# Kernel tuning notes

Hardware: AMD Instinct MI355X
Metric: run time of the kernel (lower is better)

The kernel has to match this reference:

```python
import jax, jax.numpy as jnp
import numpy as np

# ---- module constants (from init_kwargs) ----
VOXEL_SIZE = np.array([0.1, 0.1, 0.2], np.float32)
PC_RANGE = np.array([0.0, -40.0, -3.0, 70.4, 40.0, 1.0], np.float32)
MAX_PTS = 10            # max_points_in_voxel
MAX_VOX = 40000         # max_voxel_num (hard voxelization cap per sample)
GRID = np.round((PC_RANGE[3:] - PC_RANGE[:3]) / VOXEL_SIZE).astype(np.int32)  # [704,800,20] (x,y,z)
BIG = int(GRID[0]) * int(GRID[1]) * int(GRID[2])

PC_MIN = jnp.asarray(PC_RANGE[:3])
VSIZE = jnp.asarray(VOXEL_SIZE)
GRID_J = jnp.asarray(GRID)

B = 8
N_PER_B = 120000


def setup_inputs() -> dict:
    key = jax.random.key(0)
    k1, = jax.random.split(key, 1)
    u = jax.random.uniform(k1, (B * N_PER_B, 4), dtype=jnp.float32)
    # place points inside (and slightly around) pc_range
    x = u[:, 0] * 72.0 - 0.5
    y = u[:, 1] * 82.0 - 41.0
    z = u[:, 2] * 4.4 - 3.2
    inten = u[:, 3]
    bs_idx = jnp.repeat(jnp.arange(B, dtype=jnp.float32), N_PER_B)
    points = jnp.stack([bs_idx, x, y, z, inten], axis=1)  # [960000, 5]
    return {"points": points, "batch_size": B}


def _voxelize_one(pts):
    """Hard voxelization of one point cloud pts [N,4] -> fixed-size buffers.
    Faithful to first-come voxel ordering and per-voxel point caps."""
    N = pts.shape[0]
    idxs = jnp.arange(N, dtype=jnp.int32)
    xyz = pts[:, :3]
    c = jnp.floor((xyz - PC_MIN) / VSIZE).astype(jnp.int32)  # [N,3] (x,y,z)
    valid = jnp.all((c >= 0) & (c < GRID_J), axis=1)
    lid = (c[:, 2] * GRID[1] + c[:, 1]) * GRID[0] + c[:, 0]  # z-major linear id
    lid = jnp.where(valid, lid, BIG)

    order = jnp.argsort(lid)            # stable: within a voxel, original order kept
    lid_s = lid[order]
    is_new = jnp.concatenate([jnp.ones((1,), bool), lid_s[1:] != lid_s[:-1]])
    gid = jnp.cumsum(is_new.astype(jnp.int32)) - 1           # group id per sorted point
    starts = jax.lax.cummax(jnp.where(is_new, idxs, 0))      # group start position
    pos = idxs - starts                                      # rank inside its voxel

    g_lid = jax.ops.segment_min(lid_s, gid, num_segments=N)
    g_valid = g_lid < BIG
    first_orig = jax.ops.segment_min(order.astype(jnp.int32), gid, num_segments=N)
    # voxel slot = first-appearance rank (invalid/empty groups pushed to the end)
    first_key = jnp.where(g_valid, first_orig, N + idxs)
    perm = jnp.argsort(first_key)
    slot = jnp.zeros(N, jnp.int32).at[perm].set(idxs)

    pslot = slot[gid]
    keep = g_valid[gid] & (pslot < MAX_VOX) & (pos < MAX_PTS)
    sslot = jnp.where(keep, pslot, MAX_VOX)   # overflow bucket, sliced off
    spos = jnp.where(keep, pos, 0)
    voxels = jnp.zeros((MAX_VOX + 1, MAX_PTS, pts.shape[1]), pts.dtype)
    voxels = voxels.at[sslot, spos].set(pts[order])[:MAX_VOX]

    gcount = jax.ops.segment_sum(keep.astype(jnp.int32), gid, num_segments=N)
    gslot = jnp.where(g_valid & (slot < MAX_VOX), slot, MAX_VOX)
    num_points = jnp.zeros(MAX_VOX + 1, jnp.int32).at[gslot].set(gcount)[:MAX_VOX]

    cs = c[order]
    gz = jax.ops.segment_min(cs[:, 2], gid, num_segments=N)
    gy = jax.ops.segment_min(cs[:, 1], gid, num_segments=N)
    gx = jax.ops.segment_min(cs[:, 0], gid, num_segments=N)
    coors = jnp.full((MAX_VOX + 1, 3), -1, jnp.int32)
    coors = coors.at[gslot].set(jnp.stack([gz, gy, gx], axis=1))[:MAX_VOX]  # (z,y,x)
    return voxels, num_points, coors


def reference(points, batch_size):
    feats = points[:, 1:]
    n_per_b = feats.shape[0] // batch_size  # points constructed contiguously per sample
    pts = feats.reshape(batch_size, n_per_b, feats.shape[1])
    voxels_b, num_b, coors_b = jax.vmap(_voxelize_one)(pts)
    voxels = voxels_b.reshape(batch_size * MAX_VOX, MAX_PTS, feats.shape[1])
    num_points = num_b.reshape(-1)
    batch_col = jnp.repeat(jnp.arange(batch_size, dtype=jnp.int32), MAX_VOX)[:, None]
    coors_batch = jnp.concatenate([batch_col, coors_b.reshape(-1, 3)], axis=1)  # [b,z,y,x]
    grid_size = jnp.asarray(GRID)
    return voxels, num_points, coors_batch, grid_size
```

## Files before the change

### kernel.cpp

```cpp
#include <hip/hip_runtime.h>

#define NB        8
#define NPB       120000
#define NPTS      (NB * NPB)
#define MAX_PTS   10
#define MAX_VOX   40000
#define GX        704
#define GY        800
#define GZ        20
#define CELLS     (GX * GY * GZ)

#define HC2       (1 << 18)
#define HMASK2    (HC2 - 1)
#define NSLOT2    (NB * HC2)

#define TILES     469
#define TILES_PAD 512
#define MBCAP     8192
#define MTILE     2048

#define EMPTY64   0xFFFFFFFFFFFFFFFFull

#define OUT_VOX   0LL
#define OUT_NUM   12800000LL
#define OUT_COOR  13120000LL
#define OUT_GRID  14400000LL

__device__ __forceinline__ bool point_cell(const float* __restrict__ p,
                                           int& cx, int& cy, int& cz) {
    cx = (int)floorf((p[1] - 0.0f)   / 0.1f);
    cy = (int)floorf((p[2] - (-40.0f)) / 0.1f);
    cz = (int)floorf((p[3] - (-3.0f))  / 0.2f);
    return (cx >= 0) & (cx < GX) & (cy >= 0) & (cy < GY) & (cz >= 0) & (cz < GZ);
}

__device__ __forceinline__ unsigned cell_hash(int lid) {
    return (((unsigned)lid * 2654435761u) >> 14) & HMASK2;
}

__global__ void k_init(float* __restrict__ out, ulonglong2* __restrict__ slab2,
                       uint4* __restrict__ flag4, unsigned* __restrict__ mcount) {
    int t = blockIdx.x * blockDim.x + threadIdx.x;
    int stride = gridDim.x * blockDim.x;
    ulonglong2 e2; e2.x = EMPTY64; e2.y = EMPTY64;
    for (int i = t; i < NSLOT2 / 2; i += stride) slab2[i] = e2;
    uint4 z4 = make_uint4(0u, 0u, 0u, 0u);
    for (int i = t; i < NPTS / 16; i += stride) flag4[i] = z4;
    if (t < NB) mcount[t * 16] = 0u;
    if (t == 0) {
        out[OUT_GRID + 0] = 704.f;
        out[OUT_GRID + 1] = 800.f;
        out[OUT_GRID + 2] = 20.f;
    }
}

__global__ void k_insert(const float* __restrict__ pts,
                         unsigned long long* __restrict__ slabB,
                         int* __restrict__ lid32) {
    int b = blockIdx.x & 7;
    int idx = (blockIdx.x >> 3) * 256 + threadIdx.x;
    if (idx >= NPB) return;
    int g = b * NPB + idx;
    const float* p = pts + (long long)g * 5;
    int cx, cy, cz;
    if (!point_cell(p, cx, cy, cz)) { lid32[g] = -1; return; }
    int lid = (cz * GY + cy) * GX + cx;
    lid32[g] = lid;
    unsigned h = cell_hash(lid);
    unsigned long long key = ((unsigned long long)(unsigned)lid << 32)
                           | (unsigned long long)(unsigned)idx;
    unsigned long long* base = slabB + (size_t)b * HC2;
    while (true) {
        unsigned long long old = atomicMin(base + h, key);
        if (old == EMPTY64) break;
        if ((old >> 32) == (key >> 32)) break;
        if (old > key) key = old;
        h = (h + 1) & HMASK2;
    }
}

__global__ void k_mark(const ulonglong2* __restrict__ slab2,
                       unsigned char* __restrict__ flag) {
    int b = blockIdx.x & 7;
    int i = (blockIdx.x >> 3) * 256 + threadIdx.x;
    ulonglong2 v = slab2[(size_t)b * (HC2 / 2) + i];
    if (v.x != EMPTY64) flag[b * NPB + (unsigned)v.x] = 1;
    if (v.y != EMPTY64) flag[b * NPB + (unsigned)v.y] = 1;
}

__global__ void k_rankscan(const unsigned char* __restrict__ flag,
                           unsigned char* __restrict__ rank8, int* __restrict__ tileSum) {
    int b = blockIdx.x & 7;
    int tile = blockIdx.x >> 3;
    int idx = tile * 256 + threadIdx.x;
    int f = 0;
    if (idx < NPB) f = flag[b * NPB + idx];
    __shared__ int sc[256];
    sc[threadIdx.x] = f;
    __syncthreads();
    for (int off = 1; off < 256; off <<= 1) {
        int v = sc[threadIdx.x];
        if ((int)threadIdx.x >= off) v += sc[threadIdx.x - off];
        __syncthreads();
        sc[threadIdx.x] = v;
        __syncthreads();
    }
    if (idx < NPB) rank8[b * NPB + idx] = (unsigned char)(sc[threadIdx.x] - f);
    if (threadIdx.x == 255) tileSum[b * TILES_PAD + tile] = sc[255];
}

__global__ void k_finish(const float* __restrict__ pts, const int* __restrict__ lid32,
                         const unsigned char* __restrict__ flag,
                         const unsigned char* __restrict__ rank8,
                         const int* __restrict__ tileSum,
                         const unsigned long long* __restrict__ slabB,
                         float* __restrict__ out, int2* __restrict__ mlist,
                         unsigned* __restrict__ mcount) {
    int b = blockIdx.x & 7;
    int tile = blockIdx.x >> 3;
    int t = threadIdx.x;

    __shared__ int sc[256];
    __shared__ int soff[TILES_PAD];
    int v0 = (2 * t     < TILES) ? tileSum[b * TILES_PAD + 2 * t]     : 0;
    int v1 = (2 * t + 1 < TILES) ? tileSum[b * TILES_PAD + 2 * t + 1] : 0;
    int w = v0 + v1;
    sc[t] = w;
    __syncthreads();
    for (int off = 1; off < 256; off <<= 1) {
        int x = sc[t];
        if (t >= off) x += sc[t - off];
        __syncthreads();
        sc[t] = x;
        __syncthreads();
    }
    int e = sc[t] - w;
    soff[2 * t] = e;
    soff[2 * t + 1] = e + v0;
    __syncthreads();

    int idx = tile * 256 + t;
    if (idx >= NPB) return;
    int g = b * NPB + idx;
    int lid = lid32[g];
    if (lid < 0) return;

    if (flag[g]) {
        int slot = soff[idx >> 8] + (int)rank8[g];
        if (slot >= MAX_VOX) return;
        unsigned ul = (unsigned)lid;
        unsigned cx = ul % (unsigned)GX;
        unsigned tt = ul / (unsigned)GX;
        unsigned cy = tt % (unsigned)GY;
        unsigned cz = tt / (unsigned)GY;
        long long r = (long long)b * MAX_VOX + slot;
        ((float4*)(out + OUT_COOR))[r] = make_float4((float)b, (float)cz, (float)cy, (float)cx);
        out[OUT_NUM + r] = 1.f;
        const float* p = pts + (long long)g * 5;
        float4* row = (float4*)(out + OUT_VOX + r * (MAX_PTS * 4));
        row[0] = make_float4(p[1], p[2], p[3], p[4]);
        float4 zf = make_float4(0.f, 0.f, 0.f, 0.f);
        #pragma unroll
        for (int i = 1; i < MAX_PTS; i++) row[i] = zf;
    } else {
        const unsigned long long* base = slabB + (size_t)b * HC2;
        unsigned h = cell_hash(lid);
        unsigned long long cur;
        while (true) {
            cur = base[h];
            if ((unsigned)(cur >> 32) == (unsigned)lid) break;
            h = (h + 1) & HMASK2;
        }
        unsigned minidx = (unsigned)cur;
        int slot = soff[(int)minidx >> 8] + (int)rank8[b * NPB + (int)minidx];
        if (slot >= MAX_VOX) return;
        unsigned m = atomicAdd(&mcount[b * 16], 1u);
        if (m < MBCAP) mlist[(size_t)b * MBCAP + m] = make_int2(slot, idx);
    }
}

__global__ void k_multi(const float* __restrict__ pts,
                        const int2* __restrict__ mlist, const unsigned* __restrict__ mcount,
                        float* __restrict__ out) {
    int b = blockIdx.y;
    unsigned n = mcount[b * 16];
    if (n > MBCAP) n = MBCAP;
    unsigned t = blockIdx.x * blockDim.x + threadIdx.x;
    const int2* lst = mlist + (size_t)b * MBCAP;
    bool active = (t < n);
    int2 e = active ? lst[t] : make_int2(-1, -1);
    int pos = 1;
    int same = 0;
    __shared__ int2 sm[MTILE];
    for (unsigned chunk = 0; chunk < n; chunk += MTILE) {
        unsigned m = n - chunk;
        if (m > MTILE) m = MTILE;
        for (unsigned i = threadIdx.x; i < m; i += 256)
            sm[i] = lst[chunk + i];
        __syncthreads();
        if (active) {
            #pragma unroll 4
            for (unsigned j = 0; j < m; j++) {
                int2 o = sm[j];
                if (o.x == e.x) { same++; if (o.y < e.y) pos++; }
            }
        }
        __syncthreads();
    }
    if (!active) return;
    if (pos == 1) {
        int cnt = same + 1;
        out[OUT_NUM + (long long)b * MAX_VOX + e.x] =
            (float)(cnt < MAX_PTS ? cnt : MAX_PTS);
    }
    if (pos >= MAX_PTS) return;
    const float* p = pts + ((long long)b * NPB + e.y) * 5;
    ((float4*)(out + OUT_VOX))[(long long)(b * MAX_VOX + e.x) * MAX_PTS + pos] =
        make_float4(p[1], p[2], p[3], p[4]);
}

extern "C" void kernel_launch(void* const* d_in, const int* in_sizes, int n_in,
                              void* d_out, int out_size, void* d_ws, size_t ws_size,
                              hipStream_t stream) {
    const float* pts = (const float*)d_in[0];
    float* out = (float*)d_out;

    char* w = (char*)d_ws;
    unsigned long long* slabB = (unsigned long long*)w;
    w += (size_t)NSLOT2 * 8;
    unsigned char* flag = (unsigned char*)w;  w += (size_t)NPTS;
    unsigned char* rank8 = (unsigned char*)w; w += (size_t)NPTS;
    int* lid32 = (int*)w;    w += (size_t)NPTS * 4;
    int* tileSum = (int*)w;  w += (size_t)NB * TILES_PAD * 4;
    int2* mlist = (int2*)w;  w += (size_t)NB * MBCAP * 8;
    unsigned* mcount = (unsigned*)w; w += (size_t)NB * 16 * 4;

    const int PB = TILES * NB;
    k_init<<<dim3(2048), dim3(256), 0, stream>>>(out, (ulonglong2*)slabB, (uint4*)flag, mcount);
    k_insert<<<dim3(PB), dim3(256), 0, stream>>>(pts, slabB, lid32);
    k_mark<<<dim3(NB * (HC2 / 2 / 256)), dim3(256), 0, stream>>>((const ulonglong2*)slabB, flag);
    k_rankscan<<<dim3(PB), dim3(256), 0, stream>>>(flag, rank8, tileSum);
    k_finish<<<dim3(PB), dim3(256), 0, stream>>>(pts, lid32, flag, rank8, tileSum, slabB, out, mlist, mcount);
    k_multi<<<dim3(MBCAP / 256, NB), dim3(256), 0, stream>>>(pts, mlist, mcount, out);
}
```

Baseline: 174.1 us.

## Mark first-of-voxel flags during insert and fold rank scan into finish

Flags start at one, and the hash-insert kernel clears the flag of the losing point whenever two points collide on a voxel key. This removes the separate mark pass over the hash slab. The per-tile rank scan moves into the finish kernel, and a light wave-reduction kernel computes per-tile counts from packed flag bytes. Multi-point entries now record the first point index and resolve their slot through a new per-point slot table, which adds a 2-byte array write and read in exchange for dropping one kernel and the rank8 buffer.

```diff
diff --git a/kernel.cpp b/kernel.cpp
--- a/kernel.cpp
+++ b/kernel.cpp
@@ -8,7 +8,6 @@
 #define GX        704
 #define GY        800
 #define GZ        20
-#define CELLS     (GX * GY * GZ)
 
 #define HC2       (1 << 18)
 #define HMASK2    (HC2 - 1)
@@ -40,14 +39,16 @@
 
 __global__ void k_init(float* __restrict__ out, ulonglong2* __restrict__ slab2,
                        uint4* __restrict__ flag4, unsigned* __restrict__ mcount) {
-    int t = blockIdx.x * blockDim.x + threadIdx.x;
-    int stride = gridDim.x * blockDim.x;
+    int b = blockIdx.x & 7;
+    int i = (blockIdx.x >> 3) * 256 + threadIdx.x;
     ulonglong2 e2; e2.x = EMPTY64; e2.y = EMPTY64;
-    for (int i = t; i < NSLOT2 / 2; i += stride) slab2[i] = e2;
-    uint4 z4 = make_uint4(0u, 0u, 0u, 0u);
-    for (int i = t; i < NPTS / 16; i += stride) flag4[i] = z4;
-    if (t < NB) mcount[t * 16] = 0u;
-    if (t == 0) {
+    slab2[(size_t)b * (HC2 / 2) + i] = e2;
+    if (i < NPB / 16) {
+        uint4 o1; o1.x = o1.y = o1.z = o1.w = 0x01010101u;
+        flag4[b * (NPB / 16) + i] = o1;
+    }
+    if (blockIdx.x == 0 && threadIdx.x < NB) mcount[threadIdx.x * 16] = 0u;
+    if (blockIdx.x == 0 && threadIdx.x == 0) {
         out[OUT_GRID + 0] = 704.f;
         out[OUT_GRID + 1] = 800.f;
         out[OUT_GRID + 2] = 20.f;
@@ -56,14 +57,14 @@
 
 __global__ void k_insert(const float* __restrict__ pts,
                          unsigned long long* __restrict__ slabB,
-                         int* __restrict__ lid32) {
+                         int* __restrict__ lid32, unsigned char* __restrict__ flag) {
     int b = blockIdx.x & 7;
     int idx = (blockIdx.x >> 3) * 256 + threadIdx.x;
     if (idx >= NPB) return;
     int g = b * NPB + idx;
     const float* p = pts + (long long)g * 5;
     int cx, cy, cz;
-    if (!point_cell(p, cx, cy, cz)) { lid32[g] = -1; return; }
+    if (!point_cell(p, cx, cy, cz)) { lid32[g] = -1; flag[g] = 0; return; }
     int lid = (cz * GY + cy) * GX + cx;
     lid32[g] = lid;
     unsigned h = cell_hash(lid);
@@ -73,49 +74,35 @@
     while (true) {
         unsigned long long old = atomicMin(base + h, key);
         if (old == EMPTY64) break;
-        if ((old >> 32) == (key >> 32)) break;
+        if ((old >> 32) == (key >> 32)) {
+            unsigned loser = (old > key) ? (unsigned)old : (unsigned)key;
+            flag[b * NPB + (int)loser] = 0;
+            break;
+        }
         if (old > key) key = old;
         h = (h + 1) & HMASK2;
     }
 }
 
-__global__ void k_mark(const ulonglong2* __restrict__ slab2,
-                       unsigned char* __restrict__ flag) {
-    int b = blockIdx.x & 7;
-    int i = (blockIdx.x >> 3) * 256 + threadIdx.x;
-    ulonglong2 v = slab2[(size_t)b * (HC2 / 2) + i];
-    if (v.x != EMPTY64) flag[b * NPB + (unsigned)v.x] = 1;
-    if (v.y != EMPTY64) flag[b * NPB + (unsigned)v.y] = 1;
-}
-
-__global__ void k_rankscan(const unsigned char* __restrict__ flag,
-                           unsigned char* __restrict__ rank8, int* __restrict__ tileSum) {
-    int b = blockIdx.x & 7;
-    int tile = blockIdx.x >> 3;
-    int idx = tile * 256 + threadIdx.x;
-    int f = 0;
-    if (idx < NPB) f = flag[b * NPB + idx];
-    __shared__ int sc[256];
-    sc[threadIdx.x] = f;
-    __syncthreads();
-    for (int off = 1; off < 256; off <<= 1) {
-        int v = sc[threadIdx.x];
-        if ((int)threadIdx.x >= off) v += sc[threadIdx.x - off];
-        __syncthreads();
-        sc[threadIdx.x] = v;
-        __syncthreads();
-    }
-    if (idx < NPB) rank8[b * NPB + idx] = (unsigned char)(sc[threadIdx.x] - f);
-    if (threadIdx.x == 255) tileSum[b * TILES_PAD + tile] = sc[255];
+__global__ void k_count(const unsigned* __restrict__ flag32, int* __restrict__ tileSum) {
+    int w = blockIdx.x * 4 + ((int)threadIdx.x >> 6);
+    int lane = threadIdx.x & 63;
+    int b = w & 7;
+    int tile = w >> 3;
+    int i = tile * 64 + lane;
+    unsigned x = (i < NPB / 4) ? flag32[b * (NPB / 4) + i] : 0u;
+    int s = (int)((x * 0x01010101u) >> 24);
+    #pragma unroll
+    for (int off = 32; off; off >>= 1) s += __shfl_down(s, off);
+    if (lane == 0) tileSum[b * TILES_PAD + tile] = s;
 }
 
 __global__ void k_finish(const float* __restrict__ pts, const int* __restrict__ lid32,
                          const unsigned char* __restrict__ flag,
-                         const unsigned char* __restrict__ rank8,
                          const int* __restrict__ tileSum,
                          const unsigned long long* __restrict__ slabB,
-                         float* __restrict__ out, int2* __restrict__ mlist,
-                         unsigned* __restrict__ mcount) {
+                         float* __restrict__ out, unsigned short* __restrict__ slotOf,
+                         int2* __restrict__ mlist, unsigned* __restrict__ mcount) {
     int b = blockIdx.x & 7;
     int tile = blockIdx.x >> 3;
     int t = threadIdx.x;
@@ -140,13 +127,26 @@
     __syncthreads();
 
     int idx = tile * 256 + t;
+    int g = b * NPB + idx;
+    int f = (idx < NPB) ? (int)flag[g] : 0;
+    sc[t] = f;
+    __syncthreads();
+    for (int off = 1; off < 256; off <<= 1) {
+        int x = sc[t];
+        if (t >= off) x += sc[t - off];
+        __syncthreads();
+        sc[t] = x;
+        __syncthreads();
+    }
+    int rank = sc[t] - f;
+
     if (idx >= NPB) return;
-    int g = b * NPB + idx;
     int lid = lid32[g];
     if (lid < 0) return;
 
-    if (flag[g]) {
-        int slot = soff[idx >> 8] + (int)rank8[g];
+    if (f) {
+        int slot = soff[tile] + rank;
+        slotOf[g] = (unsigned short)(slot < 65535 ? slot : 65535);
         if (slot >= MAX_VOX) return;
         unsigned ul = (unsigned)lid;
         unsigned cx = ul % (unsigned)GX;
@@ -172,15 +172,14 @@
             h = (h + 1) & HMASK2;
         }
         unsigned minidx = (unsigned)cur;
-        int slot = soff[(int)minidx >> 8] + (int)rank8[b * NPB + (int)minidx];
-        if (slot >= MAX_VOX) return;
         unsigned m = atomicAdd(&mcount[b * 16], 1u);
-        if (m < MBCAP) mlist[(size_t)b * MBCAP + m] = make_int2(slot, idx);
+        if (m < MBCAP) mlist[(size_t)b * MBCAP + m] = make_int2((int)minidx, idx);
     }
 }
 
 __global__ void k_multi(const float* __restrict__ pts,
                         const int2* __restrict__ mlist, const unsigned* __restrict__ mcount,
+                        const unsigned short* __restrict__ slotOf,
                         float* __restrict__ out) {
     int b = blockIdx.y;
     unsigned n = mcount[b * 16];
@@ -208,14 +207,16 @@
         __syncthreads();
     }
     if (!active) return;
+    int slot = (int)slotOf[(size_t)b * NPB + e.x];
+    if (slot >= MAX_VOX) return;
     if (pos == 1) {
         int cnt = same + 1;
-        out[OUT_NUM + (long long)b * MAX_VOX + e.x] =
+        out[OUT_NUM + (long long)b * MAX_VOX + slot] =
             (float)(cnt < MAX_PTS ? cnt : MAX_PTS);
     }
     if (pos >= MAX_PTS) return;
     const float* p = pts + ((long long)b * NPB + e.y) * 5;
-    ((float4*)(out + OUT_VOX))[(long long)(b * MAX_VOX + e.x) * MAX_PTS + pos] =
+    ((float4*)(out + OUT_VOX))[(long long)(b * MAX_VOX + slot) * MAX_PTS + pos] =
         make_float4(p[1], p[2], p[3], p[4]);
 }
 
@@ -228,18 +229,19 @@
     char* w = (char*)d_ws;
     unsigned long long* slabB = (unsigned long long*)w;
     w += (size_t)NSLOT2 * 8;
-    unsigned char* flag = (unsigned char*)w;  w += (size_t)NPTS;
-    unsigned char* rank8 = (unsigned char*)w; w += (size_t)NPTS;
+    int2* mlist = (int2*)w;  w += (size_t)NB * MBCAP * 8;
     int* lid32 = (int*)w;    w += (size_t)NPTS * 4;
     int* tileSum = (int*)w;  w += (size_t)NB * TILES_PAD * 4;
-    int2* mlist = (int2*)w;  w += (size_t)NB * MBCAP * 8;
     unsigned* mcount = (unsigned*)w; w += (size_t)NB * 16 * 4;
+    unsigned short* slotOf = (unsigned short*)w; w += (size_t)NPTS * 2;
+    unsigned char* flag = (unsigned char*)w;  w += (size_t)NPTS;
 
     const int PB = TILES * NB;
-    k_init<<<dim3(2048), dim3(256), 0, stream>>>(out, (ulonglong2*)slabB, (uint4*)flag, mcount);
-    k_insert<<<dim3(PB), dim3(256), 0, stream>>>(pts, slabB, lid32);
-    k_mark<<<dim3(NB * (HC2 / 2 / 256)), dim3(256), 0, stream>>>((const ulonglong2*)slabB, flag);
-    k_rankscan<<<dim3(PB), dim3(256), 0, stream>>>(flag, rank8, tileSum);
-    k_finish<<<dim3(PB), dim3(256), 0, stream>>>(pts, lid32, flag, rank8, tileSum, slabB, out, mlist, mcount);
-    k_multi<<<dim3(MBCAP / 256, NB), dim3(256), 0, stream>>>(pts, mlist, mcount, out);
-}
+    k_init<<<dim3(NB * (HC2 / 2 / 256)), dim3(256), 0, stream>>>(out, (ulonglong2*)slabB,
+                                                                 (uint4*)flag, mcount);
+    k_insert<<<dim3(PB), dim3(256), 0, stream>>>(pts, slabB, lid32, flag);
+    k_count<<<dim3((TILES * NB + 3) / 4), dim3(256), 0, stream>>>((const unsigned*)flag, tileSum);
+    k_finish<<<dim3(PB), dim3(256), 0, stream>>>(pts, lid32, flag, tileSum, slabB,
+                                                 out, slotOf, mlist, mcount);
+    k_multi<<<dim3(MBCAP / 256, NB), dim3(256), 0, stream>>>(pts, mlist, mcount, slotOf, out);
+}
```

Result: no change. 172.9 us (-0.7%).
